# Kernel tuning notes

Hardware: AMD Instinct MI355X
Metric: run time of the kernel (lower is better)

The kernel has to match this reference:

```python
import jax, jax.numpy as jnp
import numpy as np

B, C_IN, C_OUT, H, W = 4, 256, 256, 64, 64
KH = KW = 3
STRIDE = 1
PAD = 1
DIL = 1


def setup_inputs() -> dict:
    key = jax.random.key(0)
    k1, k2, k3, k4 = jax.random.split(key, 4)
    x = jax.random.normal(k1, (B, C_IN, H, W), dtype=jnp.float32)
    # torchvision layout: 2*dg*KH*KW channels, (y, x) pair per kernel tap
    offset = jax.random.normal(k2, (B, 2 * KH * KW, H, W), dtype=jnp.float32)
    fan_in = C_IN * KH * KW
    weight = jax.random.normal(k3, (C_OUT, C_IN, KH, KW), dtype=jnp.float32) / np.sqrt(fan_in)
    bias = jax.random.normal(k4, (C_OUT,), dtype=jnp.float32) * 0.01
    return {"x": x, "offset": offset, "weight": weight, "bias": bias}


def _gather_bilinear_corner(x_flat, yi, xi, h, w):
    # x_flat: [B, C, H*W]; yi/xi: [B, KK, Ho, Wo] int32
    valid = ((yi >= 0) & (yi < h) & (xi >= 0) & (xi < w)).astype(x_flat.dtype)
    idx = jnp.clip(yi, 0, h - 1) * w + jnp.clip(xi, 0, w - 1)
    b = idx.shape[0]
    g = jnp.take_along_axis(x_flat, idx.reshape(b, 1, -1), axis=2)
    return g.reshape(b, x_flat.shape[1], *yi.shape[1:]), valid


def deform_conv2d(x, offset, weight, bias):
    b, c, h, w = x.shape
    o = weight.shape[0]
    kk = KH * KW
    ho = (h + 2 * PAD - DIL * (KH - 1) - 1) // STRIDE + 1
    wo = (w + 2 * PAD - DIL * (KW - 1) - 1) // STRIDE + 1

    ky = (jnp.arange(kk, dtype=jnp.float32) // KW) * DIL  # [KK]
    kx = (jnp.arange(kk, dtype=jnp.float32) % KW) * DIL
    hs = jnp.arange(ho, dtype=jnp.float32) * STRIDE - PAD   # [Ho]
    ws = jnp.arange(wo, dtype=jnp.float32) * STRIDE - PAD   # [Wo]

    off = offset.reshape(b, kk, 2, ho, wo)
    py = hs[None, None, :, None] + ky[None, :, None, None] + off[:, :, 0]  # [B,KK,Ho,Wo]
    px = ws[None, None, None, :] + kx[None, :, None, None] + off[:, :, 1]

    y0 = jnp.floor(py)
    x0 = jnp.floor(px)
    wy1 = py - y0  # fractional parts, differentiable w.r.t. offsets
    wx1 = px - x0
    wy0 = 1.0 - wy1
    wx0 = 1.0 - wx1
    y0i = y0.astype(jnp.int32)
    x0i = x0.astype(jnp.int32)

    x_flat = x.reshape(b, c, h * w)
    corners = [
        (y0i,     x0i,     wy0 * wx0),
        (y0i,     x0i + 1, wy0 * wx1),
        (y0i + 1, x0i,     wy1 * wx0),
        (y0i + 1, x0i + 1, wy1 * wx1),
    ]
    sampled = jnp.zeros((b, c, kk, ho, wo), dtype=x.dtype)
    for yi, xi, wgt in corners:
        g, valid = _gather_bilinear_corner(x_flat, yi, xi, h, w)
        sampled = sampled + g * (wgt * valid)[:, None]

    out = jnp.einsum('bckhw,ock->bohw', sampled, weight.reshape(o, c, kk))
    return out + bias[None, :, None, None]


def reference(x, offset, weight, bias):
    return deform_conv2d(x, offset, weight, bias)
```

## Files before the change

### kernel.cpp

```cpp
#include <hip/hip_runtime.h>

typedef __bf16 bf16;
typedef __bf16 bf16x4 __attribute__((ext_vector_type(4)));
typedef __bf16 bf16x8 __attribute__((ext_vector_type(8)));
typedef float  f32x4  __attribute__((ext_vector_type(4)));

#define CIN   256
#define KK    9
#define KDIM  2304
#define KITERS 72
#define PXW   32

__device__ __forceinline__ float sread(float f) {
    return __builtin_bit_cast(float,
        __builtin_amdgcn_readfirstlane(__builtin_bit_cast(int, f)));
}
__device__ __forceinline__ int sreadi(int v) {
    return __builtin_amdgcn_readfirstlane(v);
}

__global__ __launch_bounds__(256) void prep_k(const float* __restrict__ x,
                                              const float* __restrict__ w,
                                              bf16* __restrict__ xt,
                                              bf16* __restrict__ wq) {
    int bid = blockIdx.x;
    int tid = threadIdx.x;
    if (bid < 1024) {
        __shared__ bf16 tile[64][72];
        int pt = bid & 63, ct = (bid >> 6) & 3, b = bid >> 8;
        int lane = tid & 63, row = tid >> 6;
        const float* src = x + ((size_t)(b * 256 + ct * 64)) * 4096 + pt * 64;
        #pragma unroll
        for (int cc = row; cc < 64; cc += 4)
            tile[lane][cc] = (bf16)src[(size_t)cc * 4096 + lane];
        __syncthreads();
        bf16* dst = xt + ((size_t)(b * 4096 + pt * 64)) * 256 + ct * 64;
        int p = tid >> 3, j = tid & 7;
        #pragma unroll
        for (int pp = p; pp < 64; pp += 32)
            *reinterpret_cast<bf16x8*>(dst + (size_t)pp * 256 + j * 8) =
                *reinterpret_cast<const bf16x8*>(&tile[pp][j * 8]);
    } else {
        int idx  = (bid - 1024) * 256 + tid;
        int j    = idx & 7;
        int lane = (idx >> 3) & 63;
        int rest = idx >> 9;
        int kt   = rest % KITERS;
        int m    = rest / KITERS;
        int l16  = lane & 15;
        int quad = lane >> 4;
        int o    = m * 16 + l16;
        int k    = kt * 32 + quad * 8 + j;
        int tap  = k >> 8;
        int cc   = k & 255;
        wq[idx] = (bf16)w[(size_t)o * KDIM + cc * KK + tap];
    }
}

__global__ __launch_bounds__(1024, 8) void deform_gemm_k(
    const bf16*  __restrict__ xt,
    const float* __restrict__ off,
    const bf16*  __restrict__ wq,
    const float* __restrict__ bias,
    float*       __restrict__ out) {

    __shared__ bf16 S[2][PXW * 256];

    int tid   = threadIdx.x;
    int wavei = sreadi(tid >> 6);
    int lane  = tid & 63;
    int quad  = lane >> 4;
    int l16   = lane & 15;

    int bid   = blockIdx.x;
    int pb    = ((bid & 7) << 6) | (bid >> 3);
    int pix0  = pb * PXW;
    int b     = pix0 >> 12;
    int pimgb = pix0 & 4095;
    int obase = b * 73728;
    unsigned base = (unsigned)b * 1048576u + (unsigned)(lane * 4);
    int rot   = ((bid >> 3) & 1) * 4;

    f32x4 acc[2];
    acc[0] = (f32x4){0.f, 0.f, 0.f, 0.f};
    acc[1] = (f32x4){0.f, 0.f, 0.f, 0.f};

    for (int t = 0; t < KK; ++t) {
        int tap = t + rot; if (tap >= KK) tap -= KK;
        int ty = tap / 3 - 1;
        int tx = tap % 3 - 1;
        bf16* Sw = &S[t & 1][0];

        #pragma unroll
        for (int i = 0; i < 2; ++i) {
            int n    = wavei * 2 + i;
            int pimg = pimgb + n;
            float oy = off[obase + pimg + (2 * tap) * 4096];
            float ox = off[obase + pimg + (2 * tap + 1) * 4096];
            float py = (float)((pimg >> 6) + ty) + oy;
            float px = (float)((pimg & 63) + tx) + ox;
            float fy = floorf(py), fx = floorf(px);
            int   y0 = (int)fy,    x0 = (int)fx;
            float wy1 = py - fy, wx1 = px - fx;
            float wy0 = 1.f - wy1, wx0 = 1.f - wx1;
            wy0 = ((unsigned)y0       < 64u) ? wy0 : 0.f;
            wy1 = ((unsigned)(y0 + 1) < 64u) ? wy1 : 0.f;
            wx0 = ((unsigned)x0       < 64u) ? wx0 : 0.f;
            wx1 = ((unsigned)(x0 + 1) < 64u) ? wx1 : 0.f;
            int yc0 = min(max(y0, 0), 63), yc1 = min(max(y0 + 1, 0), 63);
            int xc0 = min(max(x0, 0), 63), xc1 = min(max(x0 + 1, 0), 63);
            int u0 = sreadi((yc0 * 64 + xc0) * 256);
            int u1 = sreadi((yc0 * 64 + xc1) * 256);
            int u2 = sreadi((yc1 * 64 + xc0) * 256);
            int u3 = sreadi((yc1 * 64 + xc1) * 256);
            float w0 = sread(wy0 * wx0), w1 = sread(wy0 * wx1);
            float w2 = sread(wy1 * wx0), w3 = sread(wy1 * wx1);
            bf16x4 v0 = *reinterpret_cast<const bf16x4*>(xt + base + (unsigned)u0);
            bf16x4 v1 = *reinterpret_cast<const bf16x4*>(xt + base + (unsigned)u1);
            bf16x4 v2 = *reinterpret_cast<const bf16x4*>(xt + base + (unsigned)u2);
            bf16x4 v3 = *reinterpret_cast<const bf16x4*>(xt + base + (unsigned)u3);
            float a0 = w0 * (float)v0[0] + w1 * (float)v1[0]
                     + w2 * (float)v2[0] + w3 * (float)v3[0];
            float a1 = w0 * (float)v0[1] + w1 * (float)v1[1]
                     + w2 * (float)v2[1] + w3 * (float)v3[1];
            float a2 = w0 * (float)v0[2] + w1 * (float)v1[2]
                     + w2 * (float)v2[2] + w3 * (float)v3[2];
            float a3 = w0 * (float)v0[3] + w1 * (float)v1[3]
                     + w2 * (float)v2[3] + w3 * (float)v3[3];
            bf16x4 sv;
            sv[0] = (bf16)a0; sv[1] = (bf16)a1;
            sv[2] = (bf16)a2; sv[3] = (bf16)a3;
            int gw = lane >> 1;
            int gs = (gw & 24) | ((gw ^ (n & 7)) & 7);
            *reinterpret_cast<bf16x4*>(Sw + n * 256 + gs * 8 + (lane & 1) * 4) = sv;
        }
        __syncthreads();

        const bf16* Sr  = Sw;
        const bf16* ap0 = wq + ((size_t)((wavei * KITERS + tap * 8) * 64 + lane)) * 8;
        #pragma unroll
        for (int kki = 0; kki < 8; ++kki) {
            bf16x8 a = *reinterpret_cast<const bf16x8*>(ap0 + (size_t)kki * 512);
            int g  = kki * 4 + quad;
            int gs = (g & 24) | ((g ^ (l16 & 7)) & 7);
            bf16x8 b0 = *reinterpret_cast<const bf16x8*>(Sr + l16 * 256 + gs * 8);
            bf16x8 b1 = *reinterpret_cast<const bf16x8*>(Sr + (16 + l16) * 256 + gs * 8);
            acc[0] = __builtin_amdgcn_mfma_f32_16x16x32_bf16(a, b0, acc[0], 0, 0, 0);
            acc[1] = __builtin_amdgcn_mfma_f32_16x16x32_bf16(a, b1, acc[1], 0, 0, 0);
        }
    }

    #pragma unroll
    for (int nt = 0; nt < 2; ++nt) {
        int pg   = pix0 + nt * 16 + l16;
        int bb   = pg >> 12;
        int pimg = pg & 4095;
        int m    = wavei * 16 + quad * 4;
        float* op = out + ((size_t)(bb * 256 + m)) * 4096 + pimg;
        #pragma unroll
        for (int r = 0; r < 4; ++r)
            op[(size_t)r * 4096] = acc[nt][r] + bias[m + r];
    }
}

extern "C" void kernel_launch(void* const* d_in, const int* in_sizes, int n_in,
                              void* d_out, int out_size, void* d_ws, size_t ws_size,
                              hipStream_t stream) {
    const float* x    = (const float*)d_in[0];
    const float* off  = (const float*)d_in[1];
    const float* w    = (const float*)d_in[2];
    const float* bias = (const float*)d_in[3];
    float* out = (float*)d_out;

    bf16* wq = (bf16*)d_ws;
    bf16* xt = (bf16*)((char*)d_ws + (size_t)589824 * 2);

    prep_k<<<3328, 256, 0, stream>>>(x, w, xt, wq);
    deform_gemm_k<<<512, 1024, 0, stream>>>(xt, off, wq, bias, out);
}
```

Measured before the change: 117.2 us.

## Switch GEMM to 32x32x16 MFMA with split-K across waves and LDS reduction

The GEMM stage moves from 16x16x32 MFMAs, where each wave owns 16 output channels and two 16-pixel tiles, to 32x32x16 MFMAs. Each wave now owns a 32-channel tile and half of each tap's K range, with the two K halves summed through shared memory at the end. The weight prepacking layout and the LDS swizzle are changed to match the new fragment shapes. The aim is to use the larger MFMA shape and cut the B-operand LDS reads per MFMA. In exchange it adds an extra reduction pass through LDS with two barriers, and half the waves sit idle during the output write.

Measured after the change: 121.0 us. +3.2%, slower.

```diff
diff --git a/kernel.cpp b/kernel.cpp
--- a/kernel.cpp
+++ b/kernel.cpp
@@ -4,12 +4,13 @@
 typedef __bf16 bf16x4 __attribute__((ext_vector_type(4)));
 typedef __bf16 bf16x8 __attribute__((ext_vector_type(8)));
 typedef float  f32x4  __attribute__((ext_vector_type(4)));
+typedef float  f32x16 __attribute__((ext_vector_type(16)));
 
-#define CIN   256
-#define KK    9
-#define KDIM  2304
-#define KITERS 72
-#define PXW   32
+#define CIN    256
+#define KK     9
+#define KDIM   2304
+#define KSTEPS 144
+#define PXW    32
 
 __device__ __forceinline__ float sread(float f) {
     return __builtin_bit_cast(float,
@@ -43,17 +44,15 @@
     } else {
         int idx  = (bid - 1024) * 256 + tid;
         int j    = idx & 7;
-        int lane = (idx >> 3) & 63;
+        int L    = (idx >> 3) & 63;
         int rest = idx >> 9;
-        int kt   = rest % KITERS;
-        int m    = rest / KITERS;
-        int l16  = lane & 15;
-        int quad = lane >> 4;
-        int o    = m * 16 + l16;
-        int k    = kt * 32 + quad * 8 + j;
-        int tap  = k >> 8;
-        int cc   = k & 255;
-        wq[idx] = (bf16)w[(size_t)o * KDIM + cc * KK + tap];
+        int KT   = rest % KSTEPS;
+        int mt   = rest / KSTEPS;
+        int o    = mt * 32 + (L & 31);
+        int kg   = KT * 16 + ((L >> 5) << 3) + j;
+        int tap  = kg >> 8;
+        int ch   = kg & 255;
+        wq[idx] = (bf16)w[(size_t)o * KDIM + ch * 9 + tap];
     }
 }
 
@@ -69,8 +68,10 @@
     int tid   = threadIdx.x;
     int wavei = sreadi(tid >> 6);
     int lane  = tid & 63;
-    int quad  = lane >> 4;
-    int l16   = lane & 15;
+    int px32  = lane & 31;
+    int khl   = lane >> 5;
+    int mt    = wavei & 7;
+    int kh    = wavei >> 3;
 
     int bid   = blockIdx.x;
     int pb    = ((bid & 7) << 6) | (bid >> 3);
@@ -81,9 +82,9 @@
     unsigned base = (unsigned)b * 1048576u + (unsigned)(lane * 4);
     int rot   = ((bid >> 3) & 1) * 4;
 
-    f32x4 acc[2];
-    acc[0] = (f32x4){0.f, 0.f, 0.f, 0.f};
-    acc[1] = (f32x4){0.f, 0.f, 0.f, 0.f};
+    f32x16 acc;
+    #pragma unroll
+    for (int r = 0; r < 16; ++r) acc[r] = 0.f;
 
     for (int t = 0; t < KK; ++t) {
         int tap = t + rot; if (tap >= KK) tap -= KK;
@@ -131,35 +132,48 @@
             sv[0] = (bf16)a0; sv[1] = (bf16)a1;
             sv[2] = (bf16)a2; sv[3] = (bf16)a3;
             int gw = lane >> 1;
-            int gs = (gw & 24) | ((gw ^ (n & 7)) & 7);
+            int gs = gw ^ n;
             *reinterpret_cast<bf16x4*>(Sw + n * 256 + gs * 8 + (lane & 1) * 4) = sv;
         }
         __syncthreads();
 
-        const bf16* Sr  = Sw;
-        const bf16* ap0 = wq + ((size_t)((wavei * KITERS + tap * 8) * 64 + lane)) * 8;
+        const bf16* Sr = Sw;
         #pragma unroll
-        for (int kki = 0; kki < 8; ++kki) {
-            bf16x8 a = *reinterpret_cast<const bf16x8*>(ap0 + (size_t)kki * 512);
-            int g  = kki * 4 + quad;
-            int gs = (g & 24) | ((g ^ (l16 & 7)) & 7);
-            bf16x8 b0 = *reinterpret_cast<const bf16x8*>(Sr + l16 * 256 + gs * 8);
-            bf16x8 b1 = *reinterpret_cast<const bf16x8*>(Sr + (16 + l16) * 256 + gs * 8);
-            acc[0] = __builtin_amdgcn_mfma_f32_16x16x32_bf16(a, b0, acc[0], 0, 0, 0);
-            acc[1] = __builtin_amdgcn_mfma_f32_16x16x32_bf16(a, b1, acc[1], 0, 0, 0);
+        for (int kk = 0; kk < 8; ++kk) {
+            int KT = tap * 16 + kh * 8 + kk;
+            bf16x8 a = *reinterpret_cast<const bf16x8*>(
+                wq + ((size_t)((mt * KSTEPS + KT) * 64 + lane)) * 8);
+            int g  = (kh * 8 + kk) * 2 + khl;
+            int gs = g ^ px32;
+            bf16x8 bb = *reinterpret_cast<const bf16x8*>(
+                Sr + px32 * 256 + gs * 8);
+            acc = __builtin_amdgcn_mfma_f32_32x32x16_bf16(a, bb, acc, 0, 0, 0);
         }
     }
+    __syncthreads();
 
-    #pragma unroll
-    for (int nt = 0; nt < 2; ++nt) {
-        int pg   = pix0 + nt * 16 + l16;
-        int bb   = pg >> 12;
-        int pimg = pg & 4095;
-        int m    = wavei * 16 + quad * 4;
-        float* op = out + ((size_t)(bb * 256 + m)) * 4096 + pimg;
+    float* Sf = (float*)&S[0][0];
+    if (kh == 1) {
+        float* p = Sf + (size_t)(mt * 64 + lane) * 16;
         #pragma unroll
-        for (int r = 0; r < 4; ++r)
-            op[(size_t)r * 4096] = acc[nt][r] + bias[m + r];
+        for (int q = 0; q < 4; ++q)
+            *reinterpret_cast<f32x4*>(p + q * 4) =
+                (f32x4){acc[q*4+0], acc[q*4+1], acc[q*4+2], acc[q*4+3]};
+    }
+    __syncthreads();
+
+    if (kh == 0) {
+        const float* p = Sf + (size_t)(mt * 64 + lane) * 16;
+        #pragma unroll
+        for (int r = 0; r < 16; ++r) acc[r] += p[r];
+
+        int pimg = pimgb + px32;
+        #pragma unroll
+        for (int r = 0; r < 16; ++r) {
+            int row = (r & 3) + 8 * (r >> 2) + 4 * khl;
+            int o   = mt * 32 + row;
+            out[((size_t)(b * 256 + o)) * 4096 + pimg] = acc[r] + bias[o];
+        }
     }
 }
 
```
